# Kernel optimization log

Measured on AMD Instinct MI355X. Metric: run time of the kernel, lower is better.

## Reference

```python
import jax, jax.numpy as jnp
import numpy as np

DIM = 768
HEADS = 12
HIDDEN = 3072  # int(dim * mlp_ratio)
DEGREE = 3
EPS = 1e-5


def layer_norm(x, g, b):
    m = jnp.mean(x, axis=-1, keepdims=True)
    v = jnp.mean((x - m) ** 2, axis=-1, keepdims=True)
    return (x - m) * jax.lax.rsqrt(v + EPS) * g + b


def cheby_layer(x, coeffs):
    # x: (B, N, I); coeffs: (I, O, DEGREE+1)
    t = jnp.tanh(x)
    theta = jnp.arccos(t)  # (B, N, I)
    d = jnp.arange(DEGREE + 1, dtype=x.dtype)
    basis = jnp.cos(theta[..., None] * d)  # (B, N, I, D)
    return jnp.einsum('bnid,iod->bno', basis, coeffs)


def setup_inputs() -> dict:
    key = jax.random.key(0)
    ks = jax.random.split(key, 9)
    B, N, C, H = 32, 197, DIM, HIDDEN
    x = jax.random.normal(ks[0], (B, N, C), dtype=jnp.float32)
    g1 = jnp.ones((C,), jnp.float32)
    b1 = jnp.zeros((C,), jnp.float32)
    w_qkv = jax.random.normal(ks[1], (C, 3 * C), jnp.float32) * (C ** -0.5)
    w_proj = jax.random.normal(ks[2], (C, C), jnp.float32) * (C ** -0.5)
    b_proj = jnp.zeros((C,), jnp.float32)
    g2 = jnp.ones((C,), jnp.float32)
    b2 = jnp.zeros((C,), jnp.float32)
    c1 = jax.random.normal(ks[3], (C, H, DEGREE + 1), jnp.float32) / (C * (DEGREE + 1))
    c2 = jax.random.normal(ks[4], (H, C, DEGREE + 1), jnp.float32) / (H * (DEGREE + 1))
    return {"x": x, "g1": g1, "b1": b1, "w_qkv": w_qkv, "w_proj": w_proj,
            "b_proj": b_proj, "g2": g2, "b2": b2, "c1": c1, "c2": c2}


def reference(x, g1, b1, w_qkv, w_proj, b_proj, g2, b2, c1, c2):
    B, N, C = x.shape
    hd = C // HEADS
    scale = hd ** -0.5
    # --- attention branch ---
    h = layer_norm(x, g1, b1)
    qkv = (h @ w_qkv).reshape(B, N, 3, HEADS, hd).transpose(2, 0, 3, 1, 4)
    q, k, v = qkv[0], qkv[1], qkv[2]  # (B, H, N, hd)
    attn = jax.nn.softmax(jnp.einsum('bhnd,bhmd->bhnm', q, k) * scale, axis=-1)
    o = jnp.einsum('bhnm,bhmd->bhnd', attn, v).transpose(0, 2, 1, 3).reshape(B, N, C)
    x = x + o @ w_proj + b_proj
    # --- ChebyKAN MLP branch ---
    h = layer_norm(x, g2, b2)
    h = cheby_layer(h, c1)   # (B, N, HIDDEN)
    h = cheby_layer(h, c2)   # (B, N, C)
    return x + h
```

## Files before the change

### kernel.cpp

```cpp
#include <hip/hip_runtime.h>
#include <hip/hip_bf16.h>
#include <cmath>
#include <cstdint>
#include <cstddef>

#define DEV __device__ __forceinline__

typedef __attribute__((ext_vector_type(4))) float f32x4;
typedef __attribute__((ext_vector_type(8))) short bf16x8;
typedef __attribute__((ext_vector_type(4))) unsigned int u32x4;
typedef __attribute__((ext_vector_type(4))) unsigned short u16x4;

constexpr int NBATCH = 32;
constexpr int SEQ    = 197;
constexpr int CH     = 768;
constexpr int H3     = 3 * CH;
constexpr int NHEADS = 12;
constexpr int HD     = 64;
constexpr int HID    = 3072;
constexpr int TOK    = NBATCH * SEQ;
constexpr int TOKP   = 6400;
constexpr int KSPLIT = 3;
constexpr float LNEPS = 1e-5f;

DEV unsigned short f2bf(float f) {
  unsigned int u = __builtin_bit_cast(unsigned int, f);
  u += 0x7fffu + ((u >> 16) & 1u);
  return (unsigned short)(u >> 16);
}
DEV float bf2f(unsigned short s) {
  unsigned int u = ((unsigned int)s) << 16;
  return __builtin_bit_cast(float, u);
}

DEV void async_copy16(void* lds, const void* gmem) {
  __builtin_amdgcn_global_load_lds(
      (const __attribute__((address_space(1))) unsigned int*)gmem,
      (__attribute__((address_space(3))) unsigned int*)lds, 16, 0, 0);
}

template <int POW3>
__global__ void ln_kernel(const float* __restrict__ xin, const float* __restrict__ gg,
                          const float* __restrict__ bb, unsigned short* __restrict__ outp) {
  const int row  = blockIdx.x * 4 + (threadIdx.x >> 6);
  const int lane = threadIdx.x & 63;
  const int ld   = POW3 ? 3 * CH : CH;
  if (row >= TOK) {
    u16x4 z = {0, 0, 0, 0};
    #pragma unroll
    for (int c = 0; c < 3; ++c) {
      if (POW3) {
        #pragma unroll
        for (int p = 0; p < 3; ++p)
          *(u16x4*)&outp[(size_t)row * ld + p * CH + c * 256 + lane * 4] = z;
      } else {
        *(u16x4*)&outp[(size_t)row * ld + c * 256 + lane * 4] = z;
      }
    }
    return;
  }
  f32x4 v[3];
  float s = 0.f, s2 = 0.f;
  #pragma unroll
  for (int c = 0; c < 3; ++c) {
    v[c] = *(const f32x4*)&xin[(size_t)row * CH + c * 256 + lane * 4];
    #pragma unroll
    for (int e = 0; e < 4; ++e) { s += v[c][e]; s2 += v[c][e] * v[c][e]; }
  }
  #pragma unroll
  for (int off = 32; off; off >>= 1) { s += __shfl_xor(s, off); s2 += __shfl_xor(s2, off); }
  const float mean = s * (1.f / CH);
  const float var  = s2 * (1.f / CH) - mean * mean;
  const float rs   = rsqrtf(var + LNEPS);
  #pragma unroll
  for (int c = 0; c < 3; ++c) {
    f32x4 gv = *(const f32x4*)&gg[c * 256 + lane * 4];
    f32x4 bv = *(const f32x4*)&bb[c * 256 + lane * 4];
    u16x4 o1, o2, o3;
    #pragma unroll
    for (int e = 0; e < 4; ++e) {
      float f = (v[c][e] - mean) * rs * gv[e] + bv[e];
      if (POW3) {
        f = tanhf(f);
        const float f2 = f * f, f3 = f2 * f;
        o1[e] = f2bf(f); o2[e] = f2bf(f2); o3[e] = f2bf(f3);
      } else {
        o1[e] = f2bf(f);
      }
    }
    if (POW3) {
      *(u16x4*)&outp[(size_t)row * ld + c * 256 + lane * 4]           = o1;
      *(u16x4*)&outp[(size_t)row * ld + CH + c * 256 + lane * 4]      = o2;
      *(u16x4*)&outp[(size_t)row * ld + 2 * CH + c * 256 + lane * 4]  = o3;
    } else {
      *(u16x4*)&outp[(size_t)row * ld + c * 256 + lane * 4] = o1;
    }
  }
}

__global__ void transpose_bf16(const float* __restrict__ in, unsigned short* __restrict__ outp,
                               int K, int N) {
  __shared__ unsigned short tile[64][65];
  const int k0 = blockIdx.x * 64, n0 = blockIdx.y * 64;
  const int tc = threadIdx.x & 63, tr = threadIdx.x >> 6;
  #pragma unroll
  for (int rr = 0; rr < 64; rr += 4)
    tile[rr + tr][tc] = f2bf(in[(size_t)(k0 + rr + tr) * N + n0 + tc]);
  __syncthreads();
  #pragma unroll
  for (int rr = 0; rr < 64; rr += 4)
    outp[(size_t)(n0 + rr + tr) * K + k0 + tc] = tile[tc][rr + tr];
}

__global__ void cheb_combine(const float* __restrict__ cc, unsigned short* __restrict__ outp,
                             float* __restrict__ partial, int I, int O) {
  __shared__ unsigned short t1[64][65];
  __shared__ unsigned short t2[64][65];
  __shared__ unsigned short t3[64][65];
  __shared__ float psum[4][64];
  const int i0 = blockIdx.x * 64, o0 = blockIdx.y * 64;
  const int tc = threadIdx.x & 63, tr = threadIdx.x >> 6;
  float bs = 0.f;
  #pragma unroll
  for (int rr = 0; rr < 64; rr += 4) {
    f32x4 v = *(const f32x4*)&cc[((size_t)(i0 + rr + tr) * O + (o0 + tc)) * 4];
    t1[rr + tr][tc] = f2bf(v[1] - 3.f * v[3]);
    t2[rr + tr][tc] = f2bf(2.f * v[2]);
    t3[rr + tr][tc] = f2bf(4.f * v[3]);
    bs += v[0] - v[2];
  }
  psum[tr][tc] = bs;
  __syncthreads();
  const size_t K3 = (size_t)3 * I;
  #pragma unroll
  for (int rr = 0; rr < 64; rr += 4) {
    size_t ob = (size_t)(o0 + rr + tr) * K3 + i0 + tc;
    outp[ob]         = t1[tc][rr + tr];
    outp[ob + I]     = t2[tc][rr + tr];
    outp[ob + 2 * I] = t3[tc][rr + tr];
  }
  if (tr == 0)
    partial[(size_t)blockIdx.x * O + o0 + tc] =
        psum[0][tc] + psum[1][tc] + psum[2][tc] + psum[3][tc];
}

__global__ void bias_finish(const float* __restrict__ partial, float* __restrict__ bias,
                            int nblk, int O) {
  const int o = blockIdx.x * 256 + threadIdx.x;
  float s = 0.f;
  for (int k = 0; k < nblk; ++k) s += partial[(size_t)k * O + o];
  bias[o] = s;
}

__global__ void zero_pad_rows(unsigned short* __restrict__ p) {
  const size_t idx = ((size_t)blockIdx.x * 256 + threadIdx.x) * 4;
  u16x4 z = {0, 0, 0, 0};
  *(u16x4*)&p[(size_t)TOK * CH + idx] = z;
}

template <int EPI>
__global__ __launch_bounds__(256)
void gemm_kernel(const unsigned short* __restrict__ A,
                 const unsigned short* __restrict__ BT,
                 const int Ktot, const int Nn,
                 const float* __restrict__ bias,
                 const float* __restrict__ resid,
                 void* __restrict__ Cout) {
  __shared__ __align__(16) unsigned short As[2][128 * 32];
  __shared__ __align__(16) unsigned short Bs[2][128 * 32];
  const int t = threadIdx.x;
  const int lane = t & 63;
  const int wid = t >> 6;
  const int wm = wid >> 1, wn = wid & 1;
  const int bm = blockIdx.x * 128;
  const int bn = blockIdx.y * 128;
  const int srow = t >> 2;
  const int scol = (t & 3) * 8;
  const int chunk = Ktot / gridDim.z;
  const int kbase = blockIdx.z * chunk;
  const int nkt = chunk >> 5;
  f32x4 acc[4][4] = {};

  auto stage = [&](int buf, int kt) {
    const int kk = kbase + (kt << 5);
    char* lb = (char*)&Bs[buf][0] + (wid << 10);
    async_copy16(lb,        &BT[(size_t)(bn + srow) * Ktot + kk + scol]);
    async_copy16(lb + 4096, &BT[(size_t)(bn + 64 + srow) * Ktot + kk + scol]);
    char* la = (char*)&As[buf][0] + (wid << 10);
    async_copy16(la,        &A[(size_t)(bm + srow) * Ktot + kk + scol]);
    async_copy16(la + 4096, &A[(size_t)(bm + 64 + srow) * Ktot + kk + scol]);
  };

  int cur = 0;
  stage(0, 0);
  for (int kt = 0; kt < nkt; ++kt) {
    if (kt + 1 < nkt) {
      stage(cur ^ 1, kt + 1);
      asm volatile("s_waitcnt vmcnt(4)" ::: "memory");
    } else {
      asm volatile("s_waitcnt vmcnt(0)" ::: "memory");
    }
    __builtin_amdgcn_s_barrier();
    __builtin_amdgcn_sched_barrier(0);
    bf16x8 af[4], bfr[4];
    const int frow = lane & 15;
    const int fk = (lane >> 4) * 8;
    #pragma unroll
    for (int m = 0; m < 4; ++m)
      af[m] = *(const bf16x8*)&As[cur][(wm * 64 + m * 16 + frow) * 32 + fk];
    #pragma unroll
    for (int n = 0; n < 4; ++n)
      bfr[n] = *(const bf16x8*)&Bs[cur][(wn * 64 + n * 16 + frow) * 32 + fk];
    #pragma unroll
    for (int m = 0; m < 4; ++m)
      #pragma unroll
      for (int n = 0; n < 4; ++n)
        acc[m][n] = __builtin_amdgcn_mfma_f32_16x16x32_bf16(af[m], bfr[n], acc[m][n], 0, 0, 0);
    __builtin_amdgcn_s_barrier();
    cur ^= 1;
  }
  #pragma unroll
  for (int m = 0; m < 4; ++m) {
    #pragma unroll
    for (int n = 0; n < 4; ++n) {
      #pragma unroll
      for (int r = 0; r < 4; ++r) {
        const int row = bm + wm * 64 + m * 16 + (lane >> 4) * 4 + r;
        const int col = bn + wn * 64 + n * 16 + (lane & 15);
        const float v = acc[m][n][r];
        if (EPI == 0) {
          ((unsigned short*)Cout)[(size_t)row * Nn + col] = f2bf(v);
        } else if (EPI == 1) {
          float o = 0.f;
          if (row < TOK) o = v + bias[col] + resid[(size_t)row * Nn + col];
          ((float*)Cout)[(size_t)row * Nn + col] = o;
        } else if (EPI == 2) {
          const float u = tanhf(v + bias[col]);
          const float u2 = u * u, u3 = u2 * u;
          unsigned short* o = (unsigned short*)Cout;
          const size_t b0 = (size_t)row * (3 * Nn) + col;
          o[b0]          = f2bf(u);
          o[b0 + Nn]     = f2bf(u2);
          o[b0 + 2 * Nn] = f2bf(u3);
        } else {
          ((float*)Cout)[((size_t)blockIdx.z * TOKP + row) * Nn + col] = v;
        }
      }
    }
  }
}

__global__ void cheb2_reduce(const float* __restrict__ part, const float* __restrict__ bias,
                             const float* __restrict__ resid, float* __restrict__ outp) {
  const size_t idx = ((size_t)blockIdx.x * 256 + threadIdx.x) * 4;
  const int col = (int)(idx % CH);
  f32x4 s = *(const f32x4*)&part[idx];
  #pragma unroll
  for (int z = 1; z < KSPLIT; ++z) {
    f32x4 p = *(const f32x4*)&part[(size_t)z * TOKP * CH + idx];
    #pragma unroll
    for (int e = 0; e < 4; ++e) s[e] += p[e];
  }
  const f32x4 bv = *(const f32x4*)&bias[col];
  const f32x4 rv = *(const f32x4*)&resid[idx];
  f32x4 o;
  #pragma unroll
  for (int e = 0; e < 4; ++e) o[e] = s[e] + bv[e] + rv[e];
  *(f32x4*)&outp[idx] = o;
}

__global__ __launch_bounds__(256)
void attn_kernel(const unsigned short* __restrict__ qkv, unsigned short* __restrict__ aout) {
  constexpr int VSTR = 232;
  __shared__ __align__(16) unsigned short Vlds[64 * VSTR];
  __shared__ __align__(16) unsigned short Plds[4][16 * VSTR];
  const int bh = blockIdx.x;
  const int b = bh / NHEADS, hh = bh - b * NHEADS;
  const int t = threadIdx.x, lane = t & 63, wid = t >> 6;
  const size_t base = (size_t)b * SEQ * H3;
  const int part = t & 7, key0 = t >> 3;
  for (int it = 0; it < 7; ++it) {
    const int key = key0 + it * 32;
    u32x4 raw = {0, 0, 0, 0};
    if (key < SEQ)
      raw = *(const u32x4*)&qkv[base + (size_t)key * H3 + 2 * CH + hh * HD + part * 8];
    const unsigned short* us = (const unsigned short*)&raw;
    #pragma unroll
    for (int e = 0; e < 8; ++e)
      Vlds[(part * 8 + e) * VSTR + key] = us[e];
  }
  for (int idx = t; idx < 4 * 16 * 16; idx += 256) {
    const int buf = idx >> 8, rr = (idx >> 4) & 15, ccc = idx & 15;
    Plds[buf][rr * VSTR + 208 + ccc] = 0;
  }
  __syncthreads();

  for (int qt = wid; qt < 13; qt += 4) {
    const int qrow = qt * 16 + (lane & 15);
    const size_t qbase = base + (size_t)qrow * H3 + hh * HD + (lane >> 4) * 8;
    const bf16x8 qf0 = *(const bf16x8*)&qkv[qbase];
    const bf16x8 qf1 = *(const bf16x8*)&qkv[qbase + 32];
    float sv[13][4];
    #pragma unroll
    for (int ktile = 0; ktile < 13; ++ktile) {
      const int keyc = ktile * 16 + (lane & 15);
      const size_t kbase = base + (size_t)keyc * H3 + CH + hh * HD + (lane >> 4) * 8;
      const bf16x8 kf0 = *(const bf16x8*)&qkv[kbase];
      const bf16x8 kf1 = *(const bf16x8*)&qkv[kbase + 32];
      f32x4 s = {0.f, 0.f, 0.f, 0.f};
      s = __builtin_amdgcn_mfma_f32_16x16x32_bf16(qf0, kf0, s, 0, 0, 0);
      s = __builtin_amdgcn_mfma_f32_16x16x32_bf16(qf1, kf1, s, 0, 0, 0);
      const bool valid = keyc < SEQ;
      #pragma unroll
      for (int r = 0; r < 4; ++r)
        sv[ktile][r] = valid ? s[r] * 0.125f : -INFINITY;
    }
    float rsum[4];
    #pragma unroll
    for (int r = 0; r < 4; ++r) {
      float mx = -INFINITY;
      #pragma unroll
      for (int kt2 = 0; kt2 < 13; ++kt2) mx = fmaxf(mx, sv[kt2][r]);
      #pragma unroll
      for (int off = 1; off < 16; off <<= 1) mx = fmaxf(mx, __shfl_xor(mx, off));
      float sum = 0.f;
      #pragma unroll
      for (int kt2 = 0; kt2 < 13; ++kt2) {
        const float p = __expf(sv[kt2][r] - mx);
        sv[kt2][r] = p;
        sum += p;
      }
      #pragma unroll
      for (int off = 1; off < 16; off <<= 1) sum += __shfl_xor(sum, off);
      rsum[r] = sum;
    }
    const int g4 = (lane >> 4) * 4;
    #pragma unroll
    for (int kt2 = 0; kt2 < 13; ++kt2)
      #pragma unroll
      for (int r = 0; r < 4; ++r)
        Plds[wid][(g4 + r) * VSTR + kt2 * 16 + (lane & 15)] = f2bf(sv[kt2][r]);
    asm volatile("s_waitcnt lgkmcnt(0)" ::: "memory");
    f32x4 oacc[4] = {};
    #pragma unroll
    for (int ks = 0; ks < 7; ++ks) {
      const bf16x8 pf = *(const bf16x8*)&Plds[wid][(lane & 15) * VSTR + ks * 32 + (lane >> 4) * 8];
      #pragma unroll
      for (int n = 0; n < 4; ++n) {
        const bf16x8 vf = *(const bf16x8*)&Vlds[(n * 16 + (lane & 15)) * VSTR + ks * 32 + (lane >> 4) * 8];
        oacc[n] = __builtin_amdgcn_mfma_f32_16x16x32_bf16(pf, vf, oacc[n], 0, 0, 0);
      }
    }
    #pragma unroll
    for (int n = 0; n < 4; ++n)
      #pragma unroll
      for (int r = 0; r < 4; ++r) {
        const int q = qt * 16 + g4 + r;
        if (q < SEQ) {
          const float val = oacc[n][r] / rsum[r];
          aout[(size_t)(b * SEQ + q) * CH + hh * HD + n * 16 + (lane & 15)] = f2bf(val);
        }
      }
  }
}

extern "C" void kernel_launch(void* const* d_in, const int* in_sizes, int n_in,
                              void* d_out, int out_size, void* d_ws, size_t ws_size,
                              hipStream_t stream) {
  const float* x      = (const float*)d_in[0];
  const float* g1     = (const float*)d_in[1];
  const float* b1     = (const float*)d_in[2];
  const float* w_qkv  = (const float*)d_in[3];
  const float* w_proj = (const float*)d_in[4];
  const float* b_proj = (const float*)d_in[5];
  const float* g2     = (const float*)d_in[6];
  const float* b2     = (const float*)d_in[7];
  const float* c1     = (const float*)d_in[8];
  const float* c2     = (const float*)d_in[9];

  char* ws = (char*)d_ws;
  const size_t SZ_H      = (size_t)TOKP * CH * 2;
  const size_t SZ_WQKVT  = (size_t)H3 * CH * 2;
  const size_t SZ_QKVB   = (size_t)TOKP * H3 * 2;
  const size_t SZ_AOUTB  = (size_t)TOKP * CH * 2;
  const size_t SZ_WPROJT = (size_t)CH * CH * 2;
  const size_t SZ_T2B3   = (size_t)TOKP * 3 * HID * 2;
  const size_t SZ_C1T    = (size_t)HID * 3 * CH * 2;
  const size_t SZ_T1B3   = (size_t)TOKP * 3 * CH * 2;
  const size_t SZ_PARTK  = (size_t)KSPLIT * TOKP * CH * 4;
  const size_t SZ_C2T    = (size_t)CH * 3 * HID * 2;
  const size_t SZ_XMID   = (size_t)TOKP * CH * 4;

  size_t off = 0;
  const size_t unionA = off;
  {
    size_t phase1 = SZ_H + SZ_WQKVT + SZ_QKVB + SZ_AOUTB + SZ_WPROJT;
    off += (SZ_T2B3 > phase1 ? SZ_T2B3 : phase1);
  }
  const size_t unionB = off;
  {
    size_t ab = SZ_C1T + SZ_T1B3;
    off += (SZ_PARTK > ab ? SZ_PARTK : ab);
  }
  const size_t o_c2T  = off; off += SZ_C2T;
  const size_t o_xmid = off; off += SZ_XMID;
  const size_t o_b1   = off; off += (size_t)HID * 4;
  const size_t o_b2   = off; off += (size_t)CH * 4;
  const size_t o_p1   = off; off += (size_t)(CH / 64) * HID * 4;
  const size_t o_p2   = off; off += (size_t)(HID / 64) * CH * 4;

  unsigned short* h      = (unsigned short*)(ws + unionA);
  unsigned short* wqkvT  = (unsigned short*)(ws + unionA + SZ_H);
  unsigned short* qkvb   = (unsigned short*)(ws + unionA + SZ_H + SZ_WQKVT);
  unsigned short* aoutb  = (unsigned short*)(ws + unionA + SZ_H + SZ_WQKVT + SZ_QKVB);
  unsigned short* wprojT = (unsigned short*)(ws + unionA + SZ_H + SZ_WQKVT + SZ_QKVB + SZ_AOUTB);
  unsigned short* t2b3   = (unsigned short*)(ws + unionA);
  unsigned short* c1T    = (unsigned short*)(ws + unionB);
  unsigned short* t1b3   = (unsigned short*)(ws + unionB + SZ_C1T);
  float*          partK  = (float*)(ws + unionB);
  unsigned short* c2T    = (unsigned short*)(ws + o_c2T);
  float*          xmid   = (float*)(ws + o_xmid);
  float*          bias1  = (float*)(ws + o_b1);
  float*          bias2  = (float*)(ws + o_b2);
  float*          part1  = (float*)(ws + o_p1);
  float*          part2  = (float*)(ws + o_p2);
  (void)ws_size; (void)in_sizes; (void)n_in; (void)out_size;

  transpose_bf16<<<dim3(CH / 64, H3 / 64), 256, 0, stream>>>(w_qkv, wqkvT, CH, H3);
  transpose_bf16<<<dim3(CH / 64, CH / 64), 256, 0, stream>>>(w_proj, wprojT, CH, CH);
  cheb_combine<<<dim3(CH / 64, HID / 64), 256, 0, stream>>>(c1, c1T, part1, CH, HID);
  cheb_combine<<<dim3(HID / 64, CH / 64), 256, 0, stream>>>(c2, c2T, part2, HID, CH);
  bias_finish<<<dim3(HID / 256), 256, 0, stream>>>(part1, bias1, CH / 64, HID);
  bias_finish<<<dim3(CH / 256), 256, 0, stream>>>(part2, bias2, HID / 64, CH);
  zero_pad_rows<<<dim3(72), 256, 0, stream>>>(aoutb);

  ln_kernel<0><<<dim3(TOKP / 4), 256, 0, stream>>>(x, g1, b1, h);
  gemm_kernel<0><<<dim3(TOKP / 128, H3 / 128), 256, 0, stream>>>(h, wqkvT, CH, H3,
                                                                 nullptr, nullptr, qkvb);
  attn_kernel<<<dim3(NBATCH * NHEADS), 256, 0, stream>>>(qkvb, aoutb);
  gemm_kernel<1><<<dim3(TOKP / 128, CH / 128), 256, 0, stream>>>(aoutb, wprojT, CH, CH,
                                                                 b_proj, x, xmid);
  ln_kernel<1><<<dim3(TOKP / 4), 256, 0, stream>>>(xmid, g2, b2, t1b3);
  gemm_kernel<2><<<dim3(TOKP / 128, HID / 128), 256, 0, stream>>>(t1b3, c1T, H3, HID,
                                                                  bias1, nullptr, t2b3);
  gemm_kernel<3><<<dim3(TOKP / 128, CH / 128, KSPLIT), 256, 0, stream>>>(t2b3, c2T, 3 * HID, CH,
                                                                         nullptr, nullptr, partK);
  cheb2_reduce<<<dim3(TOK * CH / 1024), 256, 0, stream>>>(partK, bias2, xmid, (float*)d_out);
}
```

Baseline: 470.9 us.

## Swizzle GEMM blocks across XCDs, use fast tanh, split cheb powers into planes

Adds an XCD-aware block-index remap to the GEMM kernel so neighbouring tiles land on the same chiplet and share L2. The tanh calls are replaced with an exp/reciprocal approximation. The second Chebyshev layer's activations and weights are stored as three separate power planes, so each K-split slice reads contiguous memory instead of a strided third of a row. The changes touch layout, scheduling and math precision together, and the fast tanh may lose accuracy for large inputs.

```diff
diff --git a/kernel.cpp b/kernel.cpp
--- a/kernel.cpp
+++ b/kernel.cpp
@@ -33,10 +33,27 @@
   return __builtin_bit_cast(float, u);
 }
 
+DEV float fast_tanh(float x) {
+  const float e = __expf(2.f * x);
+  return 1.f - 2.f * __builtin_amdgcn_rcpf(e + 1.f);
+}
+
 DEV void async_copy16(void* lds, const void* gmem) {
   __builtin_amdgcn_global_load_lds(
       (const __attribute__((address_space(1))) unsigned int*)gmem,
       (__attribute__((address_space(3))) unsigned int*)lds, 16, 0, 0);
+}
+
+DEV void xcd_swizzle(int& bx, int& by) {
+  const int gx = (int)gridDim.x;
+  const int nwg = gx * (int)gridDim.y;
+  const int flat = bx + by * gx;
+  const int q = nwg >> 3, r = nwg & 7;
+  const int xcd = flat & 7, idx = flat >> 3;
+  const int swz = (xcd < r) ? (xcd * (q + 1) + idx)
+                            : (r * (q + 1) + (xcd - r) * q + idx);
+  bx = swz % gx;
+  by = swz / gx;
 }
 
 template <int POW3>
@@ -81,7 +98,7 @@
     for (int e = 0; e < 4; ++e) {
       float f = (v[c][e] - mean) * rs * gv[e] + bv[e];
       if (POW3) {
-        f = tanhf(f);
+        f = fast_tanh(f);
         const float f2 = f * f, f3 = f2 * f;
         o1[e] = f2bf(f); o2[e] = f2bf(f2); o3[e] = f2bf(f3);
       } else {
@@ -112,6 +129,7 @@
     outp[(size_t)(n0 + rr + tr) * K + k0 + tc] = tile[tc][rr + tr];
 }
 
+template <int PSPLIT>
 __global__ void cheb_combine(const float* __restrict__ cc, unsigned short* __restrict__ outp,
                              float* __restrict__ partial, int I, int O) {
   __shared__ unsigned short t1[64][65];
@@ -131,13 +149,21 @@
   }
   psum[tr][tc] = bs;
   __syncthreads();
-  const size_t K3 = (size_t)3 * I;
   #pragma unroll
   for (int rr = 0; rr < 64; rr += 4) {
-    size_t ob = (size_t)(o0 + rr + tr) * K3 + i0 + tc;
-    outp[ob]         = t1[tc][rr + tr];
-    outp[ob + I]     = t2[tc][rr + tr];
-    outp[ob + 2 * I] = t3[tc][rr + tr];
+    if (PSPLIT == 0) {
+      const size_t K3 = (size_t)3 * I;
+      size_t ob = (size_t)(o0 + rr + tr) * K3 + i0 + tc;
+      outp[ob]         = t1[tc][rr + tr];
+      outp[ob + I]     = t2[tc][rr + tr];
+      outp[ob + 2 * I] = t3[tc][rr + tr];
+    } else {
+      const size_t plane = (size_t)O * I;
+      size_t ob = (size_t)(o0 + rr + tr) * I + i0 + tc;
+      outp[ob]             = t1[tc][rr + tr];
+      outp[ob + plane]     = t2[tc][rr + tr];
+      outp[ob + 2 * plane] = t3[tc][rr + tr];
+    }
   }
   if (tr == 0)
     partial[(size_t)blockIdx.x * O + o0 + tc] =
@@ -168,21 +194,25 @@
                  void* __restrict__ Cout) {
   __shared__ __align__(16) unsigned short As[2][128 * 32];
   __shared__ __align__(16) unsigned short Bs[2][128 * 32];
+  if (EPI == 3) {
+    A  += (size_t)blockIdx.z * TOKP * Ktot;
+    BT += (size_t)blockIdx.z * Nn * Ktot;
+  }
+  int bx = blockIdx.x, by = blockIdx.y;
+  xcd_swizzle(bx, by);
   const int t = threadIdx.x;
   const int lane = t & 63;
   const int wid = t >> 6;
   const int wm = wid >> 1, wn = wid & 1;
-  const int bm = blockIdx.x * 128;
-  const int bn = blockIdx.y * 128;
+  const int bm = bx * 128;
+  const int bn = by * 128;
   const int srow = t >> 2;
   const int scol = (t & 3) * 8;
-  const int chunk = Ktot / gridDim.z;
-  const int kbase = blockIdx.z * chunk;
-  const int nkt = chunk >> 5;
+  const int nkt = Ktot >> 5;
   f32x4 acc[4][4] = {};
 
   auto stage = [&](int buf, int kt) {
-    const int kk = kbase + (kt << 5);
+    const int kk = kt << 5;
     char* lb = (char*)&Bs[buf][0] + (wid << 10);
     async_copy16(lb,        &BT[(size_t)(bn + srow) * Ktot + kk + scol]);
     async_copy16(lb + 4096, &BT[(size_t)(bn + 64 + srow) * Ktot + kk + scol]);
@@ -235,13 +265,14 @@
           if (row < TOK) o = v + bias[col] + resid[(size_t)row * Nn + col];
           ((float*)Cout)[(size_t)row * Nn + col] = o;
         } else if (EPI == 2) {
-          const float u = tanhf(v + bias[col]);
+          const float u = fast_tanh(v + bias[col]);
           const float u2 = u * u, u3 = u2 * u;
           unsigned short* o = (unsigned short*)Cout;
-          const size_t b0 = (size_t)row * (3 * Nn) + col;
-          o[b0]          = f2bf(u);
-          o[b0 + Nn]     = f2bf(u2);
-          o[b0 + 2 * Nn] = f2bf(u3);
+          const size_t plane = (size_t)TOKP * Nn;
+          const size_t b0 = (size_t)row * Nn + col;
+          o[b0]             = f2bf(u);
+          o[b0 + plane]     = f2bf(u2);
+          o[b0 + 2 * plane] = f2bf(u3);
         } else {
           ((float*)Cout)[((size_t)blockIdx.z * TOKP + row) * Nn + col] = v;
         }
@@ -384,18 +415,18 @@
   const size_t SZ_QKVB   = (size_t)TOKP * H3 * 2;
   const size_t SZ_AOUTB  = (size_t)TOKP * CH * 2;
   const size_t SZ_WPROJT = (size_t)CH * CH * 2;
-  const size_t SZ_T2B3   = (size_t)TOKP * 3 * HID * 2;
+  const size_t SZ_UB     = (size_t)3 * TOKP * HID * 2;
   const size_t SZ_C1T    = (size_t)HID * 3 * CH * 2;
   const size_t SZ_T1B3   = (size_t)TOKP * 3 * CH * 2;
   const size_t SZ_PARTK  = (size_t)KSPLIT * TOKP * CH * 4;
-  const size_t SZ_C2T    = (size_t)CH * 3 * HID * 2;
+  const size_t SZ_C2T    = (size_t)3 * CH * HID * 2;
   const size_t SZ_XMID   = (size_t)TOKP * CH * 4;
 
   size_t off = 0;
   const size_t unionA = off;
   {
     size_t phase1 = SZ_H + SZ_WQKVT + SZ_QKVB + SZ_AOUTB + SZ_WPROJT;
-    off += (SZ_T2B3 > phase1 ? SZ_T2B3 : phase1);
+    off += (SZ_UB > phase1 ? SZ_UB : phase1);
   }
   const size_t unionB = off;
   {
@@ -414,7 +445,7 @@
   unsigned short* qkvb   = (unsigned short*)(ws + unionA + SZ_H + SZ_WQKVT);
   unsigned short* aoutb  = (unsigned short*)(ws + unionA + SZ_H + SZ_WQKVT + SZ_QKVB);
   unsigned short* wprojT = (unsigned short*)(ws + unionA + SZ_H + SZ_WQKVT + SZ_QKVB + SZ_AOUTB);
-  unsigned short* t2b3   = (unsigned short*)(ws + unionA);
+  unsigned short* ub     = (unsigned short*)(ws + unionA);
   unsigned short* c1T    = (unsigned short*)(ws + unionB);
   unsigned short* t1b3   = (unsigned short*)(ws + unionB + SZ_C1T);
   float*          partK  = (float*)(ws + unionB);
@@ -428,8 +459,8 @@
 
   transpose_bf16<<<dim3(CH / 64, H3 / 64), 256, 0, stream>>>(w_qkv, wqkvT, CH, H3);
   transpose_bf16<<<dim3(CH / 64, CH / 64), 256, 0, stream>>>(w_proj, wprojT, CH, CH);
-  cheb_combine<<<dim3(CH / 64, HID / 64), 256, 0, stream>>>(c1, c1T, part1, CH, HID);
-  cheb_combine<<<dim3(HID / 64, CH / 64), 256, 0, stream>>>(c2, c2T, part2, HID, CH);
+  cheb_combine<0><<<dim3(CH / 64, HID / 64), 256, 0, stream>>>(c1, c1T, part1, CH, HID);
+  cheb_combine<1><<<dim3(HID / 64, CH / 64), 256, 0, stream>>>(c2, c2T, part2, HID, CH);
   bias_finish<<<dim3(HID / 256), 256, 0, stream>>>(part1, bias1, CH / 64, HID);
   bias_finish<<<dim3(CH / 256), 256, 0, stream>>>(part2, bias2, HID / 64, CH);
   zero_pad_rows<<<dim3(72), 256, 0, stream>>>(aoutb);
@@ -442,8 +473,8 @@
                                                                  b_proj, x, xmid);
   ln_kernel<1><<<dim3(TOKP / 4), 256, 0, stream>>>(xmid, g2, b2, t1b3);
   gemm_kernel<2><<<dim3(TOKP / 128, HID / 128), 256, 0, stream>>>(t1b3, c1T, H3, HID,
-                                                                  bias1, nullptr, t2b3);
-  gemm_kernel<3><<<dim3(TOKP / 128, CH / 128, KSPLIT), 256, 0, stream>>>(t2b3, c2T, 3 * HID, CH,
+                                                                  bias1, nullptr, ub);
+  gemm_kernel<3><<<dim3(TOKP / 128, CH / 128, KSPLIT), 256, 0, stream>>>(ub, c2T, HID, CH,
                                                                          nullptr, nullptr, partK);
   cheb2_reduce<<<dim3(TOK * CH / 1024), 256, 0, stream>>>(partK, bias2, xmid, (float*)d_out);
 }
```

Result: slower. 498.0 us (+5.7%).
